# Kernel tuning notes

Hardware: AMD Instinct MI355X
Metric: run time of the kernel (lower is better)

The kernel has to match this reference:

```python
import jax, jax.numpy as jnp
import numpy as np

T = 0.04
PIC_NUM = 4  # images per identity (hardcoded in SP_loss)


def setup_inputs() -> dict:
    key = jax.random.key(0)
    N, D = 8192, 256  # 2048 identities x 4 images, 256-dim ReID features
    x = jax.random.normal(key, (N, D), dtype=jnp.float32)
    x = x / jnp.linalg.norm(x, axis=1, keepdims=True)  # L2-normalize (cosine sims)
    return {"x": x}


def reference(x):
    N = x.shape[0]
    G = N // PIC_NUM  # number of identity groups
    s = (x @ x.T) / T  # [N, N] scaled similarity matrix

    # Diagonal 4x4 blocks: within-class similarities. [G, 4, 4]
    d4 = s.reshape(G, PIC_NUM, G, PIC_NUM)
    gidx = jnp.arange(G)
    pos = d4[gidx, :, gidx, :]  # [G, 4, 4]

    # hard positive: -T * log( sum_{i,j in class} exp(-dot_ij / T) )  (soft-min)
    hard_pos = -T * jax.nn.logsumexp(-pos.reshape(G, PIC_NUM * PIC_NUM), axis=1)

    # least-hard positive: T * log( sum_i 1 / (sum_j exp(-dot_ij / T)) )
    lse_row = jax.nn.logsumexp(-pos, axis=2)           # [G, 4] = log sum_j exp(-dot/T)
    least_pos = T * jax.nn.logsumexp(-lse_row, axis=1)  # [G]

    # negatives: T * log( sum_{i in class, j not in class} exp(dot_ij / T) )
    col_group = jnp.arange(N) // PIC_NUM              # [N]
    same = col_group[None, :] == gidx[:, None]        # [G, N] same-class column mask
    s3 = s.reshape(G, PIC_NUM, N)
    neg_masked = jnp.where(same[:, None, :], -jnp.inf, s3)
    neg = T * jax.nn.logsumexp(neg_masked.reshape(G, PIC_NUM * N), axis=1)  # [G]

    # Original detaches all three S vectors before forming the loss.
    hard_pos = jax.lax.stop_gradient(hard_pos)
    least_pos = jax.lax.stop_gradient(least_pos)
    neg = jax.lax.stop_gradient(neg)

    # alpha: harmonic mean of (hard, least-hard) when hard >= 0, else 0
    alpha = jnp.where(hard_pos >= 0.0,
                      2.0 * least_pos * hard_pos / (hard_pos + least_pos),
                      0.0)
    margin = alpha * hard_pos + (1.0 - alpha) * least_pos
    # log(1 + exp(z)) == softplus(z), numerically stable, same math
    loss = jnp.mean(jax.nn.softplus((neg - margin) / T))
    return loss
```

## Files before the change

kernel.cpp:

```cpp
#include <hip/hip_runtime.h>
#include <math.h>


#define NROWS 8192
#define DDIM  256
#define NGRP  2048
#define NTB   128
#define NTILES (NTB * (NTB + 1) / 2)
#define TPW   4
#define NWG   (NTILES / TPW)
#define T_CONST 0.04f
#define INV_T   25.0f
#define EXP2_SCALE 36.06737602222409f
#define SCALE_QTR 0x7B7B7B7Bu

typedef __attribute__((ext_vector_type(8))) int   i32x8_t;
typedef __attribute__((ext_vector_type(4))) int   i32x4_t;
typedef __attribute__((ext_vector_type(4))) float f32x4_t;

__global__ __launch_bounds__(256) void prep_kernel(const float* __restrict__ x,
                                                   unsigned int* __restrict__ xq,
                                                   float* __restrict__ grpsum,
                                                   float* __restrict__ margin) {
    const int b = blockIdx.x;
    if (b < 512) {
#pragma unroll
        for (int it = 0; it < 4; ++it) {
            int gid = it * 131072 + b * 256 + threadIdx.x;
            float4 v = *(const float4*)(x + (size_t)gid * 4);
            int pk = __builtin_amdgcn_cvt_pk_fp8_f32(v.x * 16.f, v.y * 16.f, 0, false);
            pk = __builtin_amdgcn_cvt_pk_fp8_f32(v.z * 16.f, v.w * 16.f, pk, true);
            xq[gid] = (unsigned int)pk;
            if (it == 0 && gid < NGRP) grpsum[gid] = 0.f;
        }
        return;
    }
    const int g = (b - 512) * 4 + (threadIdx.x >> 6);
    const int lane = threadIdx.x & 63;
    const float* xr = x + (size_t)g * 4 * DDIM;
    float a[16];
#pragma unroll
    for (int k = 0; k < 16; ++k) a[k] = 0.f;
    for (int e = lane; e < DDIM; e += 64) {
        float vv[4];
        vv[0] = xr[e];
        vv[1] = xr[DDIM + e];
        vv[2] = xr[2 * DDIM + e];
        vv[3] = xr[3 * DDIM + e];
#pragma unroll
        for (int i = 0; i < 4; ++i)
#pragma unroll
            for (int j = 0; j < 4; ++j)
                a[i * 4 + j] = fmaf(vv[i], vv[j], a[i * 4 + j]);
    }
#pragma unroll
    for (int k = 0; k < 16; ++k) {
        float t = a[k];
        t += __shfl_xor(t, 32, 64);
        t += __shfl_xor(t, 16, 64);
        t += __shfl_xor(t, 8, 64);
        t += __shfl_xor(t, 4, 64);
        t += __shfl_xor(t, 2, 64);
        t += __shfl_xor(t, 1, 64);
        a[k] = t;
    }
    if (lane == 0) {
        float pos[16];
#pragma unroll
        for (int k = 0; k < 16; ++k) pos[k] = a[k] * INV_T;

        float mx = -pos[0];
#pragma unroll
        for (int k = 1; k < 16; ++k) mx = fmaxf(mx, -pos[k]);
        float se = 0.f;
#pragma unroll
        for (int k = 0; k < 16; ++k) se += __expf(-pos[k] - mx);
        float hard_pos = -T_CONST * (mx + __logf(se));

        float lse_row[4];
#pragma unroll
        for (int i = 0; i < 4; ++i) {
            float m2 = -pos[i * 4];
#pragma unroll
            for (int j = 1; j < 4; ++j) m2 = fmaxf(m2, -pos[i * 4 + j]);
            float s2 = 0.f;
#pragma unroll
            for (int j = 0; j < 4; ++j) s2 += __expf(-pos[i * 4 + j] - m2);
            lse_row[i] = m2 + __logf(s2);
        }
        float m3 = -lse_row[0];
#pragma unroll
        for (int i = 1; i < 4; ++i) m3 = fmaxf(m3, -lse_row[i]);
        float s3 = 0.f;
#pragma unroll
        for (int i = 0; i < 4; ++i) s3 += __expf(-lse_row[i] - m3);
        float least_pos = T_CONST * (m3 + __logf(s3));

        float alpha = (hard_pos >= 0.f)
                          ? (2.f * least_pos * hard_pos) / (hard_pos + least_pos)
                          : 0.f;
        margin[g] = alpha * hard_pos + (1.f - alpha) * least_pos;
    }
}

__global__ __launch_bounds__(64, 2) void gemm_exp_grpsum(const unsigned char* __restrict__ xq,
                                                         float* __restrict__ grpsum) {
    const int idx0 = blockIdx.x * TPW;
    int ti = (int)((257.0f - sqrtf(66049.0f - 8.0f * (float)idx0)) * 0.5f);
    while (ti * (257 - ti) / 2 > idx0) --ti;
    while ((ti + 1) * (256 - ti) / 2 <= idx0) ++ti;
    int tj = ti + (idx0 - ti * (257 - ti) / 2);

    const int lane = threadIdx.x;
    const int quad = lane >> 4;
    const int l16 = lane & 15;

    i32x8_t aF[2][4];
    int curTi = -1;

    for (int t = 0; t < TPW; ++t) {
        const int row0 = ti * 64;
        const int col0 = tj * 64;
        const bool diag = (ti == tj);

        if (ti != curTi) {
            curTi = ti;
#pragma unroll
            for (int ks = 0; ks < 2; ++ks)
#pragma unroll
                for (int mi = 0; mi < 4; ++mi) {
                    const unsigned char* pa =
                        xq + ((size_t)(row0 + mi * 16 + l16) << 8) + ks * 128 + quad * 32;
                    i32x4_t lo = *(const i32x4_t*)pa;
                    i32x4_t hi = *(const i32x4_t*)(pa + 16);
                    aF[ks][mi] = __builtin_shufflevector(lo, hi, 0, 1, 2, 3, 4, 5, 6, 7);
                }
        }

        f32x4_t acc[4][4];
#pragma unroll
        for (int i = 0; i < 4; ++i)
#pragma unroll
            for (int j = 0; j < 4; ++j)
                acc[i][j] = (f32x4_t){0.f, 0.f, 0.f, 0.f};

#pragma unroll
        for (int ks = 0; ks < 2; ++ks) {
            i32x8_t bF[4];
#pragma unroll
            for (int ni = 0; ni < 4; ++ni) {
                const unsigned char* pb =
                    xq + ((size_t)(col0 + ni * 16 + l16) << 8) + ks * 128 + quad * 32;
                i32x4_t lo = *(const i32x4_t*)pb;
                i32x4_t hi = *(const i32x4_t*)(pb + 16);
                bF[ni] = __builtin_shufflevector(lo, hi, 0, 1, 2, 3, 4, 5, 6, 7);
            }
#pragma unroll
            for (int mi = 0; mi < 4; ++mi)
#pragma unroll
                for (int ni = 0; ni < 4; ++ni)
                    acc[mi][ni] = __builtin_amdgcn_mfma_scale_f32_16x16x128_f8f6f4(
                        aF[ks][mi], bF[ni], acc[mi][ni],
                        0, 0,
                        0, (int)SCALE_QTR,
                        0, (int)SCALE_QTR);
        }

        const int rg0 = row0 >> 2;
        const int cg0 = col0 >> 2;
        float rowg[4] = {0.f, 0.f, 0.f, 0.f};
        float colp[4] = {0.f, 0.f, 0.f, 0.f};

        if (!diag) {
#pragma unroll
            for (int mi = 0; mi < 4; ++mi)
#pragma unroll
                for (int reg = 0; reg < 4; ++reg)
#pragma unroll
                    for (int ni = 0; ni < 4; ++ni) {
                        float e = exp2f(acc[mi][ni][reg] * EXP2_SCALE);
                        rowg[mi] += e;
                        colp[ni] += e;
                    }
        } else {
#pragma unroll
            for (int mi = 0; mi < 4; ++mi) {
                const int rgrp = mi * 4 + quad;
#pragma unroll
                for (int reg = 0; reg < 4; ++reg)
#pragma unroll
                    for (int ni = 0; ni < 4; ++ni) {
                        const int cgrp = ni * 4 + (l16 >> 2);
                        float e = (cgrp == rgrp) ? 0.f
                                                 : exp2f(acc[mi][ni][reg] * EXP2_SCALE);
                        rowg[mi] += e;
                    }
            }
        }

#pragma unroll
        for (int mi = 0; mi < 4; ++mi) {
            float v = rowg[mi];
            v += __shfl_xor(v, 1, 64);
            v += __shfl_xor(v, 2, 64);
            v += __shfl_xor(v, 4, 64);
            v += __shfl_xor(v, 8, 64);
            if (l16 == 0) atomicAdd(&grpsum[rg0 + mi * 4 + quad], v);
        }
        if (!diag) {
#pragma unroll
            for (int ni = 0; ni < 4; ++ni) {
                float v = colp[ni];
                v += __shfl_xor(v, 16, 64);
                v += __shfl_xor(v, 32, 64);
                v += __shfl_xor(v, 1, 64);
                v += __shfl_xor(v, 2, 64);
                if (quad == 0 && (l16 & 3) == 0)
                    atomicAdd(&grpsum[cg0 + ni * 4 + (l16 >> 2)], v);
            }
        }

        ++tj;
        if (tj == NTB) { ++ti; tj = ti; }
    }
}

__global__ __launch_bounds__(256) void finalize_kernel(const float* __restrict__ grpsum,
                                                       const float* __restrict__ margin,
                                                       float* __restrict__ out) {
    const int tid = threadIdx.x;
    float local = 0.f;
    for (int g = tid; g < NGRP; g += 256) {
        float z = __logf(grpsum[g]) - margin[g] * INV_T;
        float sp = (z > 30.f) ? z : log1pf(__expf(z));
        local += sp;
    }
    local += __shfl_xor(local, 1, 64);
    local += __shfl_xor(local, 2, 64);
    local += __shfl_xor(local, 4, 64);
    local += __shfl_xor(local, 8, 64);
    local += __shfl_xor(local, 16, 64);
    local += __shfl_xor(local, 32, 64);
    __shared__ float wsum[4];
    if ((tid & 63) == 0) wsum[tid >> 6] = local;
    __syncthreads();
    if (tid == 0) out[0] = (wsum[0] + wsum[1] + wsum[2] + wsum[3]) * (1.f / (float)NGRP);
}

extern "C" void kernel_launch(void* const* d_in, const int* in_sizes, int n_in,
                              void* d_out, int out_size, void* d_ws, size_t ws_size,
                              hipStream_t stream) {
    const float* x = (const float*)d_in[0];
    float* out = (float*)d_out;

    unsigned int* xq = (unsigned int*)d_ws;
    float* grpsum = (float*)((char*)d_ws + (size_t)NROWS * DDIM);
    float* margin = grpsum + NGRP;

    prep_kernel<<<1024, 256, 0, stream>>>(x, xq, grpsum, margin);
    gemm_exp_grpsum<<<NWG, 64, 0, stream>>>((const unsigned char*)xq, grpsum);
    finalize_kernel<<<1, 256, 0, stream>>>(grpsum, margin, out);
}
```

Baseline: 116.6 us.

## Prefetch next B tile during epilogue and fold exp2 scale into FP8 quantization

Loads the next tile's B fragments right after the MFMAs, so they arrive while the exp/reduction epilogue of the current tile runs. The loop is fully unrolled and uses precomputed per-lane offsets. The input is now quantized with sqrt(25*log2e) instead of 16 and the MFMA scale is set to one, so the accumulator is already in the exp2 domain and the per-element multiply before exp2 goes away. This changes the FP8 quantization range and precision and raises register pressure from holding two B fragment sets.

```diff
diff --git a/kernel.cpp b/kernel.cpp
--- a/kernel.cpp
+++ b/kernel.cpp
@@ -11,12 +11,18 @@
 #define NWG   (NTILES / TPW)
 #define T_CONST 0.04f
 #define INV_T   25.0f
-#define EXP2_SCALE 36.06737602222409f
-#define SCALE_QTR 0x7B7B7B7Bu
+#define QSCALE  6.005612043932249f
+#define SCALE_ONE 0x7F7F7F7Fu
 
 typedef __attribute__((ext_vector_type(8))) int   i32x8_t;
 typedef __attribute__((ext_vector_type(4))) int   i32x4_t;
 typedef __attribute__((ext_vector_type(4))) float f32x4_t;
+
+__device__ __forceinline__ i32x8_t ldfrag(const unsigned char* base, int off) {
+    i32x4_t lo = *(const i32x4_t*)(base + off);
+    i32x4_t hi = *(const i32x4_t*)(base + off + 16);
+    return __builtin_shufflevector(lo, hi, 0, 1, 2, 3, 4, 5, 6, 7);
+}
 
 __global__ __launch_bounds__(256) void prep_kernel(const float* __restrict__ x,
                                                    unsigned int* __restrict__ xq,
@@ -28,8 +34,8 @@
         for (int it = 0; it < 4; ++it) {
             int gid = it * 131072 + b * 256 + threadIdx.x;
             float4 v = *(const float4*)(x + (size_t)gid * 4);
-            int pk = __builtin_amdgcn_cvt_pk_fp8_f32(v.x * 16.f, v.y * 16.f, 0, false);
-            pk = __builtin_amdgcn_cvt_pk_fp8_f32(v.z * 16.f, v.w * 16.f, pk, true);
+            int pk = __builtin_amdgcn_cvt_pk_fp8_f32(v.x * QSCALE, v.y * QSCALE, 0, false);
+            pk = __builtin_amdgcn_cvt_pk_fp8_f32(v.z * QSCALE, v.w * QSCALE, pk, true);
             xq[gid] = (unsigned int)pk;
             if (it == 0 && gid < NGRP) grpsum[gid] = 0.f;
         }
@@ -115,26 +121,32 @@
     const int quad = lane >> 4;
     const int l16 = lane & 15;
 
+    int voff[8];
+#pragma unroll
+    for (int z = 0; z < 8; ++z)
+        voff[z] = (((z & 3) * 16 + l16) << 8) + (z >> 2) * 128 + quad * 32;
+
     i32x8_t aF[2][4];
     int curTi = -1;
 
+    i32x8_t bF[2][4];
+    {
+        const unsigned char* bb = xq + ((size_t)tj << 14);
+#pragma unroll
+        for (int z = 0; z < 8; ++z) bF[z >> 2][z & 3] = ldfrag(bb, voff[z]);
+    }
+
+#pragma unroll
     for (int t = 0; t < TPW; ++t) {
-        const int row0 = ti * 64;
-        const int col0 = tj * 64;
         const bool diag = (ti == tj);
+        const int rg0 = ti * 16;
+        const int cg0 = tj * 16;
 
         if (ti != curTi) {
             curTi = ti;
-#pragma unroll
-            for (int ks = 0; ks < 2; ++ks)
-#pragma unroll
-                for (int mi = 0; mi < 4; ++mi) {
-                    const unsigned char* pa =
-                        xq + ((size_t)(row0 + mi * 16 + l16) << 8) + ks * 128 + quad * 32;
-                    i32x4_t lo = *(const i32x4_t*)pa;
-                    i32x4_t hi = *(const i32x4_t*)(pa + 16);
-                    aF[ks][mi] = __builtin_shufflevector(lo, hi, 0, 1, 2, 3, 4, 5, 6, 7);
-                }
+            const unsigned char* ab = xq + ((size_t)ti << 14);
+#pragma unroll
+            for (int z = 0; z < 8; ++z) aF[z >> 2][z & 3] = ldfrag(ab, voff[z]);
         }
 
         f32x4_t acc[4][4];
@@ -145,29 +157,26 @@
                 acc[i][j] = (f32x4_t){0.f, 0.f, 0.f, 0.f};
 
 #pragma unroll
-        for (int ks = 0; ks < 2; ++ks) {
-            i32x8_t bF[4];
-#pragma unroll
-            for (int ni = 0; ni < 4; ++ni) {
-                const unsigned char* pb =
-                    xq + ((size_t)(col0 + ni * 16 + l16) << 8) + ks * 128 + quad * 32;
-                i32x4_t lo = *(const i32x4_t*)pb;
-                i32x4_t hi = *(const i32x4_t*)(pb + 16);
-                bF[ni] = __builtin_shufflevector(lo, hi, 0, 1, 2, 3, 4, 5, 6, 7);
-            }
+        for (int ks = 0; ks < 2; ++ks)
 #pragma unroll
             for (int mi = 0; mi < 4; ++mi)
 #pragma unroll
                 for (int ni = 0; ni < 4; ++ni)
                     acc[mi][ni] = __builtin_amdgcn_mfma_scale_f32_16x16x128_f8f6f4(
-                        aF[ks][mi], bF[ni], acc[mi][ni],
+                        aF[ks][mi], bF[ks][ni], acc[mi][ni],
                         0, 0,
-                        0, (int)SCALE_QTR,
-                        0, (int)SCALE_QTR);
-        }
-
-        const int rg0 = row0 >> 2;
-        const int cg0 = col0 >> 2;
+                        0, (int)SCALE_ONE,
+                        0, (int)SCALE_ONE);
+
+        const int ptj = tj;  (void)ptj;
+        ++tj;
+        if (tj == NTB) { ++ti; tj = ti; }
+        if (t + 1 < TPW) {
+            const unsigned char* bb = xq + ((size_t)tj << 14);
+#pragma unroll
+            for (int z = 0; z < 8; ++z) bF[z >> 2][z & 3] = ldfrag(bb, voff[z]);
+        }
+
         float rowg[4] = {0.f, 0.f, 0.f, 0.f};
         float colp[4] = {0.f, 0.f, 0.f, 0.f};
 
@@ -175,26 +184,25 @@
 #pragma unroll
             for (int mi = 0; mi < 4; ++mi)
 #pragma unroll
-                for (int reg = 0; reg < 4; ++reg)
-#pragma unroll
-                    for (int ni = 0; ni < 4; ++ni) {
-                        float e = exp2f(acc[mi][ni][reg] * EXP2_SCALE);
-                        rowg[mi] += e;
-                        colp[ni] += e;
-                    }
+                for (int ni = 0; ni < 4; ++ni) {
+                    float s4 = exp2f(acc[mi][ni][0]) + exp2f(acc[mi][ni][1])
+                             + exp2f(acc[mi][ni][2]) + exp2f(acc[mi][ni][3]);
+                    rowg[mi] += s4;
+                    colp[ni] += s4;
+                }
         } else {
 #pragma unroll
             for (int mi = 0; mi < 4; ++mi) {
                 const int rgrp = mi * 4 + quad;
 #pragma unroll
-                for (int reg = 0; reg < 4; ++reg)
-#pragma unroll
-                    for (int ni = 0; ni < 4; ++ni) {
-                        const int cgrp = ni * 4 + (l16 >> 2);
-                        float e = (cgrp == rgrp) ? 0.f
-                                                 : exp2f(acc[mi][ni][reg] * EXP2_SCALE);
-                        rowg[mi] += e;
+                for (int ni = 0; ni < 4; ++ni) {
+                    const int cgrp = ni * 4 + (l16 >> 2);
+                    if (cgrp != rgrp) {
+                        float s4 = exp2f(acc[mi][ni][0]) + exp2f(acc[mi][ni][1])
+                                 + exp2f(acc[mi][ni][2]) + exp2f(acc[mi][ni][3]);
+                        rowg[mi] += s4;
                     }
+                }
             }
         }
 
@@ -219,9 +227,6 @@
                     atomicAdd(&grpsum[cg0 + ni * 4 + (l16 >> 2)], v);
             }
         }
-
-        ++tj;
-        if (tj == NTB) { ++ti; tj = ti; }
     }
 }
 
```

Result: faster. 109.9 us (-5.8%).
